# Performance work log

Measured on AMD Instinct MI355X. Metric: run time of the kernel, lower is better.

## Reference

```python
import jax, jax.numpy as jnp
import numpy as np

EPS = 1e-8  # torch F.cosine_similarity default eps


def _reliability_map(hard, conf, pseudo_feat, num_classes):
    """Per-(batch,class) confidence-weighted centers + per-pixel cosine sim.

    hard:        [b, H, W] int class assignment defining the segments
    conf:        [b, 1, H, W] per-pixel confidence weights
    pseudo_feat: [b, d, H, W] features
    returns      [b, H, W] cosine similarity of each pixel feature to the
                 weighted-mean center of its assigned class.
    """
    b = hard.shape[0]
    onehot = jax.nn.one_hot(hard, num_classes, dtype=pseudo_feat.dtype)  # [b,H,W,c]
    weighted = pseudo_feat * conf                                        # [b,d,H,W]
    # segment-sum of weighted features per class -> [b,c,d]
    sums = jnp.einsum('bhwc,bdhw->bcd', onehot, weighted)
    counts = onehot.sum(axis=(1, 2))                                     # [b,c]
    # (class_feat * class_conf).mean(dim=1) over the n_i member pixels
    centers = sums / jnp.maximum(counts, 1.0)[..., None]                 # [b,c,d]
    # gather each pixel's class center
    cen_px = centers[jnp.arange(b)[:, None, None], hard]                 # [b,H,W,d]
    feat_px = jnp.transpose(pseudo_feat, (0, 2, 3, 1))                   # [b,H,W,d]
    num = jnp.sum(feat_px * cen_px, axis=-1)
    fn = jnp.maximum(jnp.linalg.norm(feat_px, axis=-1), EPS)
    cn = jnp.maximum(jnp.linalg.norm(cen_px, axis=-1), EPS)
    return num / (fn * cn)                                               # [b,H,W]


def _ce_per_pixel(logits, labels):
    # CrossEntropyLoss(reduction='none'), no class weights
    logp = jax.nn.log_softmax(logits, axis=1)                            # [b,c,H,W]
    picked = jnp.take_along_axis(logp, labels[:, None], axis=1)[:, 0]    # [b,H,W]
    return -picked


def reference(pred_main, pred_aux, feat_main, feat_aux):
    c = pred_main.shape[1]
    # --- no_grad block (stop_gradient) ---
    pm = jax.lax.stop_gradient(pred_main)
    pa = jax.lax.stop_gradient(pred_aux)
    fm = jax.lax.stop_gradient(feat_main)
    fa = jax.lax.stop_gradient(feat_aux)

    hard_main = jnp.argmax(pm, axis=1)                                   # [b,H,W]
    hard_aux = jnp.argmax(pa, axis=1)
    conf_main = jnp.max(jax.nn.softmax(pm, axis=1), axis=1, keepdims=True)  # [b,1,H,W]
    conf_aux = jnp.max(jax.nn.softmax(pa, axis=1), axis=1, keepdims=True)

    conf_mask = conf_main >= conf_aux                                    # [b,1,H,W]
    pseudo_label = jnp.where(conf_mask[:, 0], hard_main, hard_aux)       # [b,H,W]
    pseudo_feature = jnp.where(conf_mask, fm, fa)                        # [b,d,H,W]

    rel_main = _reliability_map(hard_main, conf_main, pseudo_feature, c)
    rel_aux = _reliability_map(hard_aux, conf_aux, pseudo_feature, c)
    # --- end no_grad ---

    ce_main = _ce_per_pixel(pred_main, pseudo_label)
    ce_aux = _ce_per_pixel(pred_aux, pseudo_label)

    loss_main = jnp.sum(ce_main * rel_aux) / jnp.sum(rel_aux)
    loss_aux = jnp.sum(ce_aux * rel_main) / jnp.sum(rel_main)
    return loss_main + loss_aux


def setup_inputs() -> dict:
    key = jax.random.key(0)
    k1, k2, k3, k4 = jax.random.split(key, 4)
    b, c, d, H, W = 4, 4, 32, 512, 512
    return {
        'pred_main': jax.random.normal(k1, (b, c, H, W), dtype=jnp.float32),
        'pred_aux': jax.random.normal(k2, (b, c, H, W), dtype=jnp.float32),
        'feat_main': jax.random.normal(k3, (b, d, H, W), dtype=jnp.float32),
        'feat_aux': jax.random.normal(k4, (b, d, H, W), dtype=jnp.float32),
    }
```

## Files before the change

kernel.cpp:

```cpp
#include <hip/hip_runtime.h>
#include <math.h>

#define HW 262144
#define NB 4
#define NC 4
#define ND 32
#define NPIX (NB * HW)
#define NG 262144
#define EPSF 1e-8f

#define OFF_SUMS    0
#define OFF_COUNTS  1024
#define OFF_CENTERS 1056
#define OFF_CNORM   2080
#define OFF_PART    2112
#define HDR_BYTES   9472
#define OFF_REC     HDR_BYTES
#define OFF_CPK     (OFF_REC + 4L * NG)
#define OFF_CEM     (OFF_CPK + 16L * NG)
#define OFF_CEA     (OFF_CEM + 16L * NG)

#define ELEM(v,e) ((e)==0?(v).x:(e)==1?(v).y:(e)==2?(v).z:(v).w)
#define W32(q,i)  ((i)==0?(q).x:(i)==1?(q).y:(i)==2?(q).z:(q).w)

__device__ __forceinline__ float wave_sum64(float v) {
#pragma unroll
  for (int off = 32; off > 0; off >>= 1) v += __shfl_xor(v, off, 64);
  return v;
}
__device__ __forceinline__ unsigned short f2bf(float f) {
  unsigned u = __float_as_uint(f);
  return (unsigned short)((u + 0x7fffu + ((u >> 16) & 1u)) >> 16);
}

__global__ __launch_bounds__(256) void passA2s(
    const float* __restrict__ pm, const float* __restrict__ pa,
    unsigned* __restrict__ recu, uint4* __restrict__ cpk4,
    float4* __restrict__ cem4, float4* __restrict__ cea4) {
  int p4 = blockIdx.x * 256 + threadIdx.x;
  int b = p4 >> 16;
  int px4 = p4 & 0xFFFF;
  const float4* xb = (const float4*)pm + (((long)b * NC) << 16) + px4;
  const float4* yb = (const float4*)pa + (((long)b * NC) << 16) + px4;
  float4 X0 = xb[0], X1 = xb[1 << 16], X2 = xb[2 << 16], X3 = xb[3 << 16];
  float4 Y0 = yb[0], Y1 = yb[1 << 16], Y2 = yb[2 << 16], Y3 = yb[3 << 16];
  float4 cem, cea;
  uint4 cpk;
  unsigned ru = 0;
#pragma unroll
  for (int e = 0; e < 4; ++e) {
    float x0 = ELEM(X0, e), x1 = ELEM(X1, e), x2 = ELEM(X2, e), x3 = ELEM(X3, e);
    float y0 = ELEM(Y0, e), y1 = ELEM(Y1, e), y2 = ELEM(Y2, e), y3 = ELEM(Y3, e);
    int hm = 0; float bm = x0;
    if (x1 > bm) { bm = x1; hm = 1; }
    if (x2 > bm) { bm = x2; hm = 2; }
    if (x3 > bm) { bm = x3; hm = 3; }
    int ha = 0; float ba = y0;
    if (y1 > ba) { ba = y1; ha = 1; }
    if (y2 > ba) { ba = y2; ha = 2; }
    if (y3 > ba) { ba = y3; ha = 3; }
    float sem = expf(x0 - bm) + expf(x1 - bm) + expf(x2 - bm) + expf(x3 - bm);
    float sea = expf(y0 - ba) + expf(y1 - ba) + expf(y2 - ba) + expf(y3 - ba);
    float confm = 1.0f / sem, confa = 1.0f / sea;
    int mk = (confm >= confa) ? 1 : 0;
    int lab = mk ? hm : ha;
    float xl = lab == 0 ? x0 : lab == 1 ? x1 : lab == 2 ? x2 : x3;
    float yl = lab == 0 ? y0 : lab == 1 ? y1 : lab == 2 ? y2 : y3;
    float vem = bm - xl + logf(sem);
    float vea = ba - yl + logf(sea);
    unsigned pk = (unsigned)f2bf(confm) | ((unsigned)f2bf(confa) << 16);
    if (e == 0) { cem.x = vem; cea.x = vea; cpk.x = pk; }
    if (e == 1) { cem.y = vem; cea.y = vea; cpk.y = pk; }
    if (e == 2) { cem.z = vem; cea.z = vea; cpk.z = pk; }
    if (e == 3) { cem.w = vem; cea.w = vea; cpk.w = pk; }
    ru |= (unsigned)(hm | (ha << 2) | (mk << 4)) << (8 * e);
  }
  cem4[p4] = cem; cea4[p4] = cea; cpk4[p4] = cpk; recu[p4] = ru;
}

__global__ __launch_bounds__(256) void countK(const unsigned* __restrict__ recu,
                                              float* __restrict__ counts) {
  int b = blockIdx.y;
  int t = blockIdx.x * 256 + threadIdx.x;
  float c[8];
#pragma unroll
  for (int j = 0; j < 8; ++j) c[j] = 0.f;
#pragma unroll
  for (int k = 0; k < 8; ++k) {
    unsigned ru = recu[(b << 16) + t + k * 8192];
#pragma unroll
    for (int e = 0; e < 4; ++e) {
      unsigned r = (ru >> (8 * e)) & 0xffu;
      int hm = r & 3, ha = (r >> 2) & 3;
      c[0] += hm == 0 ? 1.f : 0.f; c[1] += hm == 1 ? 1.f : 0.f;
      c[2] += hm == 2 ? 1.f : 0.f; c[3] += hm == 3 ? 1.f : 0.f;
      c[4] += ha == 0 ? 1.f : 0.f; c[5] += ha == 1 ? 1.f : 0.f;
      c[6] += ha == 2 ? 1.f : 0.f; c[7] += ha == 3 ? 1.f : 0.f;
    }
  }
  int lane = threadIdx.x & 63;
#pragma unroll
  for (int j = 0; j < 8; ++j) {
    float v = wave_sum64(c[j]);
    if (lane == 0) atomicAdd(&counts[(j >> 2) * 16 + b * 4 + (j & 3)], v);
  }
}

__global__ __launch_bounds__(256, 2) void fusedBsum2(
    const float* __restrict__ fm, const float* __restrict__ fa,
    const unsigned* __restrict__ recu, const uint4* __restrict__ cpk4,
    float* __restrict__ sums) {
  __shared__ float lred[4][256];
  int p4 = blockIdx.x * 256 + threadIdx.x;
  int b = blockIdx.x >> 8;
  int px4 = p4 & 0xFFFF;
  int wave = threadIdx.x >> 6, lane = threadIdx.x & 63;
  bool b0 = lane & 1, b1 = lane & 2, b2 = lane & 4;

  unsigned ru = recu[p4];
  uint4 ck = cpk4[p4];
  int mk0 = (ru >> 4) & 1, mk1 = (ru >> 12) & 1;
  int mk2 = (ru >> 20) & 1, mk3 = (ru >> 28) & 1;
  float wmw[4][4], waw[4][4];
#pragma unroll
  for (int e = 0; e < 4; ++e) {
    unsigned r = (ru >> (8 * e)) & 0xffu;
    unsigned pk = W32(ck, e);
    int hm = r & 3, ha = (r >> 2) & 3;
    float cm = __uint_as_float(pk << 16);
    float ca = __uint_as_float(pk & 0xffff0000u);
#pragma unroll
    for (int c = 0; c < 4; ++c) {
      wmw[e][c] = (hm == c) ? cm : 0.f;
      waw[e][c] = (ha == c) ? ca : 0.f;
    }
  }

  const float4* fmb = (const float4*)fm + (((long)(b * ND)) << 16) + px4;
  const float4* fab = (const float4*)fa + (((long)(b * ND)) << 16) + px4;

#pragma unroll 8
  for (int d = 0; d < ND; ++d) {
    float4 vm = fmb[(long)d << 16];
    float4 va = fab[(long)d << 16];
    float ps0 = mk0 ? vm.x : va.x;
    float ps1 = mk1 ? vm.y : va.y;
    float ps2 = mk2 ? vm.z : va.z;
    float ps3 = mk3 ? vm.w : va.w;
    float v0 = fmaf(wmw[0][0], ps0, fmaf(wmw[1][0], ps1, fmaf(wmw[2][0], ps2, wmw[3][0] * ps3)));
    float v1 = fmaf(wmw[0][1], ps0, fmaf(wmw[1][1], ps1, fmaf(wmw[2][1], ps2, wmw[3][1] * ps3)));
    float v2 = fmaf(wmw[0][2], ps0, fmaf(wmw[1][2], ps1, fmaf(wmw[2][2], ps2, wmw[3][2] * ps3)));
    float v3 = fmaf(wmw[0][3], ps0, fmaf(wmw[1][3], ps1, fmaf(wmw[2][3], ps2, wmw[3][3] * ps3)));
    float v4 = fmaf(waw[0][0], ps0, fmaf(waw[1][0], ps1, fmaf(waw[2][0], ps2, waw[3][0] * ps3)));
    float v5 = fmaf(waw[0][1], ps0, fmaf(waw[1][1], ps1, fmaf(waw[2][1], ps2, waw[3][1] * ps3)));
    float v6 = fmaf(waw[0][2], ps0, fmaf(waw[1][2], ps1, fmaf(waw[2][2], ps2, waw[3][2] * ps3)));
    float v7 = fmaf(waw[0][3], ps0, fmaf(waw[1][3], ps1, fmaf(waw[2][3], ps2, waw[3][3] * ps3)));
    float w0 = (b0 ? v1 : v0) + __shfl_xor(b0 ? v0 : v1, 1, 64);
    float w1 = (b0 ? v3 : v2) + __shfl_xor(b0 ? v2 : v3, 1, 64);
    float w2 = (b0 ? v5 : v4) + __shfl_xor(b0 ? v4 : v5, 1, 64);
    float w3 = (b0 ? v7 : v6) + __shfl_xor(b0 ? v6 : v7, 1, 64);
    float x0 = (b1 ? w1 : w0) + __shfl_xor(b1 ? w0 : w1, 2, 64);
    float x1 = (b1 ? w3 : w2) + __shfl_xor(b1 ? w2 : w3, 2, 64);
    float y = (b2 ? x1 : x0) + __shfl_xor(b2 ? x0 : x1, 4, 64);
    y += __shfl_xor(y, 8, 64);
    y += __shfl_xor(y, 16, 64);
    y += __shfl_xor(y, 32, 64);
    if (lane < 8) lred[wave][d * 8 + lane] = y;
  }
  __syncthreads();
  {
    int t = threadIdx.x;
    float v = lred[0][t] + lred[1][t] + lred[2][t] + lred[3][t];
    int d = t >> 3, j = t & 7;
    int map = j >> 2, cls = j & 3;
    atomicAdd(&sums[((map * NB + b) * NC + cls) * ND + d], v);
  }
}

__global__ __launch_bounds__(1024) void passC(
    const float* __restrict__ sums, const float* __restrict__ counts,
    float* __restrict__ centers, float* __restrict__ cnorm) {
  int t = threadIdx.x;
  int g = t >> 5;
  float cv = sums[t] / fmaxf(counts[g], 1.f);
  centers[t] = cv;
  float s = cv * cv;
#pragma unroll
  for (int off = 16; off > 0; off >>= 1) s += __shfl_xor(s, off, 32);
  if ((t & 31) == 0) cnorm[g] = fmaxf(sqrtf(s), EPSF);
}

__global__ __launch_bounds__(256) void passDf32(
    const float* __restrict__ fm, const float* __restrict__ fa,
    const unsigned* __restrict__ recu, const float4* __restrict__ cem4,
    const float4* __restrict__ cea4, const float* __restrict__ centers,
    const float* __restrict__ cnorm, float* __restrict__ part) {
  __shared__ float sc[1024];
  __shared__ float scn[32];
  __shared__ float red[4][4];
  for (int i = threadIdx.x; i < 1024; i += 256) {
    int d = i & 31, cls = (i >> 5) & 3, bb = (i >> 7) & 3, mp = i >> 9;
    sc[d * 32 + mp * 16 + bb * 4 + cls] = centers[i];
  }
  if (threadIdx.x < 32) scn[threadIdx.x] = cnorm[threadIdx.x];
  __syncthreads();

  int p4 = blockIdx.x * 256 + threadIdx.x;
  int b = p4 >> 16;
  int px4 = p4 & 0xFFFF;
  unsigned ru = recu[p4];
  int im[4], ia[4], mk[4];
#pragma unroll
  for (int e = 0; e < 4; ++e) {
    unsigned r = (ru >> (8 * e)) & 0xffu;
    im[e] = b * 4 + (r & 3);
    ia[e] = 16 + b * 4 + ((r >> 2) & 3);
    mk[e] = (r >> 4) & 1;
  }
  const float4* fmb = (const float4*)fm + (((long)(b * ND)) << 16) + px4;
  const float4* fab = (const float4*)fa + (((long)(b * ND)) << 16) + px4;
  float4 nm = {0.f, 0.f, 0.f, 0.f}, na = {0.f, 0.f, 0.f, 0.f},
         fn2 = {0.f, 0.f, 0.f, 0.f};
#pragma unroll 16
  for (int d = 0; d < ND; ++d) {
    float4 vm = fmb[(long)d << 16];
    float4 va = fab[(long)d << 16];
#pragma unroll
    for (int e = 0; e < 4; ++e) {
      float ps = mk[e] ? ELEM(vm, e) : ELEM(va, e);
      float cim = sc[d * 32 + im[e]];
      float cia = sc[d * 32 + ia[e]];
      if (e == 0) { nm.x = fmaf(ps, cim, nm.x); na.x = fmaf(ps, cia, na.x); fn2.x = fmaf(ps, ps, fn2.x); }
      if (e == 1) { nm.y = fmaf(ps, cim, nm.y); na.y = fmaf(ps, cia, na.y); fn2.y = fmaf(ps, ps, fn2.y); }
      if (e == 2) { nm.z = fmaf(ps, cim, nm.z); na.z = fmaf(ps, cia, na.z); fn2.z = fmaf(ps, ps, fn2.z); }
      if (e == 3) { nm.w = fmaf(ps, cim, nm.w); na.w = fmaf(ps, cia, na.w); fn2.w = fmaf(ps, ps, fn2.w); }
    }
  }
  float4 cem = cem4[p4], cea = cea4[p4];
  float s0 = 0.f, s1 = 0.f, s2 = 0.f, s3 = 0.f;
#pragma unroll
  for (int e = 0; e < 4; ++e) {
    float fn = fmaxf(sqrtf(ELEM(fn2, e)), EPSF);
    float rm = ELEM(nm, e) / (fn * scn[im[e]]);
    float ra = ELEM(na, e) / (fn * scn[ia[e]]);
    s0 = fmaf(ELEM(cem, e), ra, s0);
    s1 += ra;
    s2 = fmaf(ELEM(cea, e), rm, s2);
    s3 += rm;
  }
  s0 = wave_sum64(s0); s1 = wave_sum64(s1);
  s2 = wave_sum64(s2); s3 = wave_sum64(s3);
  int wave = threadIdx.x >> 6, lane = threadIdx.x & 63;
  if (lane == 0) { red[wave][0] = s0; red[wave][1] = s1; red[wave][2] = s2; red[wave][3] = s3; }
  __syncthreads();
  if (threadIdx.x < 4) {
    float v = red[0][threadIdx.x] + red[1][threadIdx.x] +
              red[2][threadIdx.x] + red[3][threadIdx.x];
    atomicAdd(&part[(blockIdx.x & 63) * 4 + threadIdx.x], v);
  }
}

__global__ __launch_bounds__(64) void passE(const float* __restrict__ part,
                                            float* __restrict__ out) {
  int t = threadIdx.x;
  float a0 = part[t * 4 + 0], a1 = part[t * 4 + 1];
  float a2 = part[t * 4 + 2], a3 = part[t * 4 + 3];
  a0 = wave_sum64(a0); a1 = wave_sum64(a1);
  a2 = wave_sum64(a2); a3 = wave_sum64(a3);
  if (t == 0) out[0] = a0 / a1 + a2 / a3;
}

extern "C" void kernel_launch(void* const* d_in, const int* in_sizes, int n_in,
                              void* d_out, int out_size, void* d_ws, size_t ws_size,
                              hipStream_t stream) {
  const float* pm = (const float*)d_in[0];
  const float* pa = (const float*)d_in[1];
  const float* fm = (const float*)d_in[2];
  const float* fa = (const float*)d_in[3];

  float* wsf = (float*)d_ws;
  float* sums = wsf + OFF_SUMS;
  float* counts = wsf + OFF_COUNTS;
  float* centers = wsf + OFF_CENTERS;
  float* cnorm = wsf + OFF_CNORM;
  float* part = wsf + OFF_PART;
  char* wsb = (char*)d_ws;
  unsigned* recu = (unsigned*)(wsb + OFF_REC);
  uint4* cpk4 = (uint4*)(wsb + OFF_CPK);
  float4* cem4 = (float4*)(wsb + OFF_CEM);
  float4* cea4 = (float4*)(wsb + OFF_CEA);

  hipMemsetAsync(d_ws, 0, HDR_BYTES, stream);
  passA2s<<<1024, 256, 0, stream>>>(pm, pa, recu, cpk4, cem4, cea4);
  countK<<<dim3(32, 4), 256, 0, stream>>>(recu, counts);
  fusedBsum2<<<1024, 256, 0, stream>>>(fm, fa, recu, cpk4, sums);
  passC<<<1, 1024, 0, stream>>>(sums, counts, centers, cnorm);
  passDf32<<<1024, 256, 0, stream>>>(fm, fa, recu, cem4, cea4, centers,
                                     cnorm, part);
  passE<<<1, 64, 0, stream>>>(part, (float*)d_out);
}
```

Before: 171.8 us.

## Restructure segment-sum kernel to accumulate over pixels per feature-dim slice

The class-sum kernel is reorganized so each block handles a 4-dim slice of features for one batch and loops over 4 pixel groups, accumulating per-class sums in registers before one cross-lane reduction. Previously every block covered all 32 dims for its pixels and ran a full shuffle reduction plus shared-memory write for each dim. This cuts shuffle and reduction work per loaded element and lets each thread keep more independent loads in flight. In exchange, the per-pixel label and confidence records are re-read once per dim slice (8 times), and the grid grows to 2048 blocks with more register accumulators per thread.

```diff
diff --git a/kernel.cpp b/kernel.cpp
--- a/kernel.cpp
+++ b/kernel.cpp
@@ -106,55 +106,68 @@
   }
 }
 
-__global__ __launch_bounds__(256, 2) void fusedBsum2(
+__global__ __launch_bounds__(256, 2) void passB4(
     const float* __restrict__ fm, const float* __restrict__ fa,
     const unsigned* __restrict__ recu, const uint4* __restrict__ cpk4,
     float* __restrict__ sums) {
-  __shared__ float lred[4][256];
-  int p4 = blockIdx.x * 256 + threadIdx.x;
-  int b = blockIdx.x >> 8;
-  int px4 = p4 & 0xFFFF;
+  __shared__ float lred[4][32];
+  int b = blockIdx.y >> 3;
+  int dp = blockIdx.y & 7;
+  int d0 = dp * 4;
   int wave = threadIdx.x >> 6, lane = threadIdx.x & 63;
   bool b0 = lane & 1, b1 = lane & 2, b2 = lane & 4;
 
-  unsigned ru = recu[p4];
-  uint4 ck = cpk4[p4];
-  int mk0 = (ru >> 4) & 1, mk1 = (ru >> 12) & 1;
-  int mk2 = (ru >> 20) & 1, mk3 = (ru >> 28) & 1;
-  float wmw[4][4], waw[4][4];
-#pragma unroll
-  for (int e = 0; e < 4; ++e) {
-    unsigned r = (ru >> (8 * e)) & 0xffu;
-    unsigned pk = W32(ck, e);
-    int hm = r & 3, ha = (r >> 2) & 3;
-    float cm = __uint_as_float(pk << 16);
-    float ca = __uint_as_float(pk & 0xffff0000u);
-#pragma unroll
-    for (int c = 0; c < 4; ++c) {
-      wmw[e][c] = (hm == c) ? cm : 0.f;
-      waw[e][c] = (ha == c) ? ca : 0.f;
+  const float4* fmP = (const float4*)fm + (((long)(b * ND + d0)) << 16);
+  const float4* faP = (const float4*)fa + (((long)(b * ND + d0)) << 16);
+  const unsigned* ruP = recu + ((long)b << 16);
+  const uint4* ckP = cpk4 + ((long)b << 16);
+
+  float acc[8][4];
+#pragma unroll
+  for (int c = 0; c < 8; ++c)
+#pragma unroll
+    for (int j = 0; j < 4; ++j) acc[c][j] = 0.f;
+
+#pragma unroll 1
+  for (int k = 0; k < 4; ++k) {
+    int g = blockIdx.x * 1024 + k * 256 + threadIdx.x;
+    unsigned ru = ruP[g];
+    uint4 ck = ckP[g];
+    float4 vm0 = fmP[g];              float4 va0 = faP[g];
+    float4 vm1 = fmP[g + (1 << 16)];  float4 va1 = faP[g + (1 << 16)];
+    float4 vm2 = fmP[g + (2 << 16)];  float4 va2 = faP[g + (2 << 16)];
+    float4 vm3 = fmP[g + (3 << 16)];  float4 va3 = faP[g + (3 << 16)];
+#pragma unroll
+    for (int e = 0; e < 4; ++e) {
+      unsigned r = (ru >> (8 * e)) & 0xffu;
+      unsigned pk = W32(ck, e);
+      int hm = r & 3, ha = (r >> 2) & 3, mk = (r >> 4) & 1;
+      float cm = __uint_as_float(pk << 16);
+      float ca = __uint_as_float(pk & 0xffff0000u);
+      float p0 = mk ? ELEM(vm0, e) : ELEM(va0, e);
+      float p1 = mk ? ELEM(vm1, e) : ELEM(va1, e);
+      float p2 = mk ? ELEM(vm2, e) : ELEM(va2, e);
+      float p3 = mk ? ELEM(vm3, e) : ELEM(va3, e);
+#pragma unroll
+      for (int c = 0; c < 4; ++c) {
+        float wm = (hm == c) ? cm : 0.f;
+        float wa = (ha == c) ? ca : 0.f;
+        acc[c][0] = fmaf(wm, p0, acc[c][0]);
+        acc[c][1] = fmaf(wm, p1, acc[c][1]);
+        acc[c][2] = fmaf(wm, p2, acc[c][2]);
+        acc[c][3] = fmaf(wm, p3, acc[c][3]);
+        acc[4 + c][0] = fmaf(wa, p0, acc[4 + c][0]);
+        acc[4 + c][1] = fmaf(wa, p1, acc[4 + c][1]);
+        acc[4 + c][2] = fmaf(wa, p2, acc[4 + c][2]);
+        acc[4 + c][3] = fmaf(wa, p3, acc[4 + c][3]);
+      }
     }
   }
 
-  const float4* fmb = (const float4*)fm + (((long)(b * ND)) << 16) + px4;
-  const float4* fab = (const float4*)fa + (((long)(b * ND)) << 16) + px4;
-
-#pragma unroll 8
-  for (int d = 0; d < ND; ++d) {
-    float4 vm = fmb[(long)d << 16];
-    float4 va = fab[(long)d << 16];
-    float ps0 = mk0 ? vm.x : va.x;
-    float ps1 = mk1 ? vm.y : va.y;
-    float ps2 = mk2 ? vm.z : va.z;
-    float ps3 = mk3 ? vm.w : va.w;
-    float v0 = fmaf(wmw[0][0], ps0, fmaf(wmw[1][0], ps1, fmaf(wmw[2][0], ps2, wmw[3][0] * ps3)));
-    float v1 = fmaf(wmw[0][1], ps0, fmaf(wmw[1][1], ps1, fmaf(wmw[2][1], ps2, wmw[3][1] * ps3)));
-    float v2 = fmaf(wmw[0][2], ps0, fmaf(wmw[1][2], ps1, fmaf(wmw[2][2], ps2, wmw[3][2] * ps3)));
-    float v3 = fmaf(wmw[0][3], ps0, fmaf(wmw[1][3], ps1, fmaf(wmw[2][3], ps2, wmw[3][3] * ps3)));
-    float v4 = fmaf(waw[0][0], ps0, fmaf(waw[1][0], ps1, fmaf(waw[2][0], ps2, waw[3][0] * ps3)));
-    float v5 = fmaf(waw[0][1], ps0, fmaf(waw[1][1], ps1, fmaf(waw[2][1], ps2, waw[3][1] * ps3)));
-    float v6 = fmaf(waw[0][2], ps0, fmaf(waw[1][2], ps1, fmaf(waw[2][2], ps2, waw[3][2] * ps3)));
-    float v7 = fmaf(waw[0][3], ps0, fmaf(waw[1][3], ps1, fmaf(waw[2][3], ps2, waw[3][3] * ps3)));
+#pragma unroll
+  for (int j = 0; j < 4; ++j) {
+    float v0 = acc[0][j], v1 = acc[1][j], v2 = acc[2][j], v3 = acc[3][j];
+    float v4 = acc[4][j], v5 = acc[5][j], v6 = acc[6][j], v7 = acc[7][j];
     float w0 = (b0 ? v1 : v0) + __shfl_xor(b0 ? v0 : v1, 1, 64);
     float w1 = (b0 ? v3 : v2) + __shfl_xor(b0 ? v2 : v3, 1, 64);
     float w2 = (b0 ? v5 : v4) + __shfl_xor(b0 ? v4 : v5, 1, 64);
@@ -165,15 +178,15 @@
     y += __shfl_xor(y, 8, 64);
     y += __shfl_xor(y, 16, 64);
     y += __shfl_xor(y, 32, 64);
-    if (lane < 8) lred[wave][d * 8 + lane] = y;
+    if (lane < 8) lred[wave][j * 8 + lane] = y;
   }
   __syncthreads();
-  {
+  if (threadIdx.x < 32) {
     int t = threadIdx.x;
     float v = lred[0][t] + lred[1][t] + lred[2][t] + lred[3][t];
-    int d = t >> 3, j = t & 7;
-    int map = j >> 2, cls = j & 3;
-    atomicAdd(&sums[((map * NB + b) * NC + cls) * ND + d], v);
+    int dj = t >> 3, bin = t & 7;
+    int map = bin >> 2, cls = bin & 3;
+    atomicAdd(&sums[((map * NB + b) * NC + cls) * ND + d0 + dj], v);
   }
 }
 
@@ -293,7 +306,7 @@
   hipMemsetAsync(d_ws, 0, HDR_BYTES, stream);
   passA2s<<<1024, 256, 0, stream>>>(pm, pa, recu, cpk4, cem4, cea4);
   countK<<<dim3(32, 4), 256, 0, stream>>>(recu, counts);
-  fusedBsum2<<<1024, 256, 0, stream>>>(fm, fa, recu, cpk4, sums);
+  passB4<<<dim3(64, 32), 256, 0, stream>>>(fm, fa, recu, cpk4, sums);
   passC<<<1, 1024, 0, stream>>>(sums, counts, centers, cnorm);
   passDf32<<<1024, 256, 0, stream>>>(fm, fa, recu, cem4, cea4, centers,
                                      cnorm, part);
```

Result: faster. 165.3 us (-3.8%).
